# Kernel optimization log

Measured on AMD Instinct MI355X. Metric: run time of the kernel, lower is better.

Reference implementation:

```python
import jax, jax.numpy as jnp
import numpy as np

ROPE_BASE = 10000.0
NEG = -1e9

def _rope_tables(N, head_dim, dtype):
    # freq buffer: angles[pos, i] = pos / base^(2i/head_dim), i over half dim
    inv = 1.0 / (ROPE_BASE ** (jnp.arange(0, head_dim, 2, dtype=jnp.float32) / head_dim))
    ang = jnp.arange(N, dtype=jnp.float32)[:, None] * inv[None, :]  # (N, hd/2)
    return jnp.cos(ang).astype(dtype), jnp.sin(ang).astype(dtype)

def _apply_rope(t, cos, sin):
    # t: (B, h, N, hd); rotate-half style
    hd = t.shape[-1]
    t1, t2 = t[..., : hd // 2], t[..., hd // 2 :]
    c = cos[None, None]  # (1,1,N,hd/2)
    s = sin[None, None]
    return jnp.concatenate([t1 * c - t2 * s, t1 * s + t2 * c], axis=-1)


def setup_inputs() -> dict:
    key = jax.random.key(0)
    B, N, D, h = 2, 2048, 2048, 16
    ks = jax.random.split(key, 5)
    x = jax.random.normal(ks[0], (B, N, D), dtype=jnp.float32)
    Wqkv = jax.random.normal(ks[1], (3 * D, D), dtype=jnp.float32) * 0.02
    Wproj = jax.random.normal(ks[2], (D, D), dtype=jnp.float32) * 0.02
    bproj = jax.random.normal(ks[3], (D,), dtype=jnp.float32) * 0.02
    L = jax.random.randint(ks[4], (B,), 1, N + 1, dtype=jnp.int32)
    return {"x": x, "Wqkv": Wqkv, "Wproj": Wproj, "bproj": bproj, "L": L, "n_heads": 16}


def reference(x, Wqkv, Wproj, bproj, L, n_heads):
    B, N, D = x.shape
    hd = D // n_heads
    scale = 1.0 / jnp.sqrt(jnp.asarray(hd, dtype=x.dtype))

    # fused QKV projection (no bias)
    qkv = jnp.einsum('bnd,ed->bne', x, Wqkv)  # (B, N, 3D)
    q, k, v = jnp.split(qkv, 3, axis=-1)
    # (B, N, h*hd) -> (B, h, N, hd)
    def heads(t):
        return t.reshape(B, N, n_heads, hd).transpose(0, 2, 1, 3)
    q, k, v = heads(q), heads(k), heads(v)

    cos, sin = _rope_tables(N, hd, x.dtype)
    q = _apply_rope(q, cos, sin)
    k = _apply_rope(k, cos, sin)

    # causal + key-padding mask (pos < L valid)
    pos = jnp.arange(N)
    causal = pos[:, None] >= pos[None, :]                    # (N, N)
    key_valid = pos[None, :] < L[:, None]                    # (B, N)
    mask = causal[None, None] & key_valid[:, None, None, :]  # (B,1,N,N)

    scores = jnp.einsum('bhqd,bhkd->bhqk', q, k) * scale
    scores = jnp.where(mask, scores, NEG)
    attn = jax.nn.softmax(scores, axis=-1)
    out = jnp.einsum('bhqk,bhkd->bhqd', attn, v)             # (B,h,N,hd)
    out = out.transpose(0, 2, 1, 3).reshape(B, N, D)
    return jnp.einsum('bnd,ed->bne', out, Wproj) + bproj
```

## Files before the change

kernel.cpp:

```cpp
#include <hip/hip_runtime.h>
#include <hip/hip_bf16.h>


typedef unsigned short u16;
typedef short bf16x8 __attribute__((ext_vector_type(8)));
typedef unsigned short u16x8 __attribute__((ext_vector_type(8)));
typedef float f32x4 __attribute__((ext_vector_type(4)));

#define MFMA16(a, b, c) __builtin_amdgcn_mfma_f32_16x16x32_bf16((a), (b), (c), 0, 0, 0)

__device__ __forceinline__ float b2f(u16 u) { return __uint_as_float(((unsigned)u) << 16); }
__device__ __forceinline__ u16 f2b(float f) {
    unsigned x = __float_as_uint(f);
    return (u16)((x + 0x7fffu + ((x >> 16) & 1u)) >> 16);
}
__device__ __forceinline__ void gload16(const u16* g, u16* lds) {
    __builtin_amdgcn_global_load_lds((__attribute__((address_space(1))) void*)g,
                                     (__attribute__((address_space(3))) void*)lds,
                                     16, 0, 0);
}

__global__ __launch_bounds__(256) void cvt_bf16(const float* __restrict__ in,
                                                u16* __restrict__ out) {
    size_t i = (size_t)blockIdx.x * 256 + threadIdx.x;
    float4 a = ((const float4*)in)[2 * i];
    float4 b = ((const float4*)in)[2 * i + 1];
    u16x8 o;
    o[0] = f2b(a.x); o[1] = f2b(a.y); o[2] = f2b(a.z); o[3] = f2b(a.w);
    o[4] = f2b(b.x); o[5] = f2b(b.y); o[6] = f2b(b.z); o[7] = f2b(b.w);
    ((u16x8*)out)[i] = o;
}

__global__ __launch_bounds__(256) void rope_tables_k(float* __restrict__ cosT,
                                                     float* __restrict__ sinT) {
    int idx = blockIdx.x * 256 + threadIdx.x;
    int n = idx >> 6, i = idx & 63;
    float inv = powf(10000.0f, -(float)(2 * i) / 128.0f);
    float ang = (float)n * inv;
    cosT[idx] = cosf(ang);
    sinT[idx] = sinf(ang);
}

template <int OUTF32>
__global__ __launch_bounds__(256, 2) void gemm_nt(const u16* __restrict__ A,
                                                  const u16* __restrict__ B,
                                                  void* __restrict__ Cv,
                                                  const float* __restrict__ bias,
                                                  int M, int Ncols, int K) {
    __shared__ u16 As[128 * 64];
    __shared__ u16 Bs[128 * 64];
    const int tx = threadIdx.x;
    const int w = tx >> 6, l = tx & 63;
    const int fr = l & 15, fg = l >> 4;
    const int wr = w >> 1, wc = w & 1;
    const long row0 = (long)blockIdx.x * 128;
    const long col0 = (long)blockIdx.y * 128;
    f32x4 acc[4][4] = {};
    const int nk = K >> 6;
    int rs[4], ss[4];
#pragma unroll
    for (int i = 0; i < 4; ++i) {
        int c = i * 256 + tx;
        rs[i] = c >> 3;
        ss[i] = (c & 7) ^ ((c >> 3) & 7);
    }
    for (int kt = 0; kt < nk; ++kt) {
        const long k0 = (long)kt << 6;
        __syncthreads();
#pragma unroll
        for (int i = 0; i < 4; ++i)
            gload16(A + (row0 + rs[i]) * K + k0 + ss[i] * 8, &As[(i * 256 + w * 64) * 8]);
#pragma unroll
        for (int i = 0; i < 4; ++i)
            gload16(B + (col0 + rs[i]) * K + k0 + ss[i] * 8, &Bs[(i * 256 + w * 64) * 8]);
        __syncthreads();
#pragma unroll
        for (int kk = 0; kk < 2; ++kk) {
            bf16x8 af[4], bfv[4];
#pragma unroll
            for (int m = 0; m < 4; ++m) {
                int r = wr * 64 + m * 16 + fr;
                af[m] = *(const bf16x8*)&As[r * 64 + (((kk * 4 + fg) ^ (r & 7)) << 3)];
            }
#pragma unroll
            for (int n = 0; n < 4; ++n) {
                int r = wc * 64 + n * 16 + fr;
                bfv[n] = *(const bf16x8*)&Bs[r * 64 + (((kk * 4 + fg) ^ (r & 7)) << 3)];
            }
#pragma unroll
            for (int m = 0; m < 4; ++m)
#pragma unroll
                for (int n = 0; n < 4; ++n) acc[m][n] = MFMA16(af[m], bfv[n], acc[m][n]);
        }
    }
#pragma unroll
    for (int m = 0; m < 4; ++m) {
#pragma unroll
        for (int n = 0; n < 4; ++n) {
#pragma unroll
            for (int r = 0; r < 4; ++r) {
                long row = row0 + wr * 64 + m * 16 + fg * 4 + r;
                long col = col0 + wc * 64 + n * 16 + fr;
                float v = acc[m][n][r];
                if (OUTF32) {
                    ((float*)Cv)[row * Ncols + col] = v + bias[col];
                } else {
                    ((u16*)Cv)[row * Ncols + col] = f2b(v);
                }
            }
        }
    }
}

__global__ __launch_bounds__(256) void rope_transpose_k(
    const u16* __restrict__ qkv, const float* __restrict__ cosT,
    const float* __restrict__ sinT, u16* __restrict__ Q, u16* __restrict__ Ko,
    u16* __restrict__ VT) {
    const int bh = blockIdx.y, b = bh >> 4, h = bh & 15;
    const int n0 = blockIdx.x << 7;
    const int tx = threadIdx.x;
    __shared__ u16 vbuf[128][136];
    const float SCALE = 0.08838834764831844f;
#pragma unroll
    for (int pass = 0; pass < 4; ++pass) {
        const int rr = pass * 32 + (tx >> 3);
        const int p = tx & 7;
        const int n = n0 + rr;
        const u16* src = qkv + ((size_t)(b * 2048 + n)) * 6144 + h * 128;
        float c[8], s[8];
#pragma unroll
        for (int j = 0; j < 8; ++j) {
            c[j] = cosT[n * 64 + p * 8 + j];
            s[j] = sinT[n * 64 + p * 8 + j];
        }
        {
            u16x8 t1 = *(const u16x8*)&src[p * 8];
            u16x8 t2 = *(const u16x8*)&src[64 + p * 8];
            u16x8 o1, o2;
#pragma unroll
            for (int j = 0; j < 8; ++j) {
                float a = b2f(t1[j]), bb = b2f(t2[j]);
                o1[j] = f2b((a * c[j] - bb * s[j]) * SCALE);
                o2[j] = f2b((a * s[j] + bb * c[j]) * SCALE);
            }
            u16* dst = Q + ((size_t)bh * 2048 + n) * 128;
            *(u16x8*)&dst[p * 8] = o1;
            *(u16x8*)&dst[64 + p * 8] = o2;
        }
        {
            u16x8 t1 = *(const u16x8*)&src[2048 + p * 8];
            u16x8 t2 = *(const u16x8*)&src[2048 + 64 + p * 8];
            u16x8 o1, o2;
#pragma unroll
            for (int j = 0; j < 8; ++j) {
                float a = b2f(t1[j]), bb = b2f(t2[j]);
                o1[j] = f2b(a * c[j] - bb * s[j]);
                o2[j] = f2b(a * s[j] + bb * c[j]);
            }
            u16* dst = Ko + ((size_t)bh * 2048 + n) * 128;
            *(u16x8*)&dst[p * 8] = o1;
            *(u16x8*)&dst[64 + p * 8] = o2;
        }
    }
#pragma unroll
    for (int i = 0; i < 8; ++i) {
        int cid = i * 256 + tx;
        int rr = cid >> 4, cc = cid & 15;
        *(u16x8*)&vbuf[rr][cc * 8] =
            *(const u16x8*)&qkv[((size_t)(b * 2048 + n0 + rr)) * 6144 + 4096 + h * 128 + cc * 8];
    }
    __syncthreads();
#pragma unroll
    for (int i = 0; i < 8; ++i) {
        int cid = i * 256 + tx;
        int j = cid >> 4, nc = cid & 15;
        u16x8 o;
#pragma unroll
        for (int e = 0; e < 8; ++e) o[e] = vbuf[nc * 8 + e][j];
        *(u16x8*)&VT[((size_t)bh * 128 + j) * 2048 + n0 + nc * 8] = o;
    }
}

__global__ __launch_bounds__(256, 2) void attn_k(const u16* __restrict__ Q,
                                                 const u16* __restrict__ K,
                                                 const u16* __restrict__ VT,
                                                 u16* __restrict__ O,
                                                 const int* __restrict__ L) {
    const int bh = blockIdx.y, b = bh >> 4, h = bh & 15;
    const int qx = blockIdx.x;
    const int qb0 = qx << 6, qb1 = (31 - qx) << 6;
    const int tx = threadIdx.x;
    const int w = tx >> 6, l = tx & 63;
    const int fr = l & 15, fg = l >> 4;
    const int Lb = L[b];
    __shared__ u16 Ks[2][64 * 128];
    __shared__ u16 Vs[2][128 * 64];
    __shared__ u16 Ps[4][16 * 72];
    const u16* Qh = Q + (size_t)bh * 2048 * 128;
    const u16* Kh = K + (size_t)bh * 2048 * 128;
    const u16* Vh = VT + (size_t)bh * 128 * 2048;
    bf16x8 aq0[4], aq1[4];
#pragma unroll
    for (int kc = 0; kc < 4; ++kc) {
        aq0[kc] = *(const bf16x8*)&Qh[(size_t)(qb0 + w * 16 + fr) * 128 + kc * 32 + fg * 8];
        aq1[kc] = *(const bf16x8*)&Qh[(size_t)(qb1 + w * 16 + fr) * 128 + kc * 32 + fg * 8];
    }
    f32x4 accO0[8] = {}, accO1[8] = {};
    float mr0[4] = {-1e30f, -1e30f, -1e30f, -1e30f};
    float mr1[4] = {-1e30f, -1e30f, -1e30f, -1e30f};
    float sr0[4] = {0.f, 0.f, 0.f, 0.f};
    float sr1[4] = {0.f, 0.f, 0.f, 0.f};
    const int kmax = min(qb1 + 63, Lb - 1);
    const int nkt = (kmax >> 6) + 1;

    auto stage_tile = [&](int kt0, int buf) {
#pragma unroll
        for (int i = 0; i < 4; ++i) {
            int c = i * 256 + tx;
            int row = c >> 4, cp = c & 15;
            gload16(Kh + (size_t)(kt0 + row) * 128 + ((cp ^ (row & 7)) << 3),
                    &Ks[buf][(i * 256 + w * 64) * 8]);
        }
#pragma unroll
        for (int i = 0; i < 4; ++i) {
            int c = i * 256 + tx;
            int row = c >> 3, cp = c & 7;
            gload16(Vh + (size_t)row * 2048 + kt0 + ((cp ^ (row & 7)) << 3),
                    &Vs[buf][(i * 256 + w * 64) * 8]);
        }
    };

    auto do_strip = [&](const bf16x8 (&aqs)[4], float (&mr)[4], float (&sr)[4],
                        f32x4 (&aO)[8], int qgb, int kt0, const u16* Ksb,
                        const u16* Vsb) {
        f32x4 accS[4];
#pragma unroll
        for (int st = 0; st < 4; ++st) {
            f32x4 z = {0.f, 0.f, 0.f, 0.f};
            accS[st] = z;
            int key = st * 16 + fr;
#pragma unroll
            for (int kc = 0; kc < 4; ++kc) {
                bf16x8 bk = *(const bf16x8*)&Ksb[key * 128 + (((kc * 4 + fg) ^ (key & 7)) << 3)];
                accS[st] = MFMA16(aqs[kc], bk, accS[st]);
            }
        }
        float sv[4][4];
#pragma unroll
        for (int st = 0; st < 4; ++st)
#pragma unroll
            for (int r = 0; r < 4; ++r) {
                int key = kt0 + st * 16 + fr;
                int qg = qgb + fg * 4 + r;
                sv[st][r] = (key <= qg && key < Lb) ? accS[st][r] : -1e30f;
            }
        float alpha[4], pr[4][4];
#pragma unroll
        for (int r = 0; r < 4; ++r) {
            float lm = fmaxf(fmaxf(sv[0][r], sv[1][r]), fmaxf(sv[2][r], sv[3][r]));
            lm = fmaxf(lm, __shfl_xor(lm, 1));
            lm = fmaxf(lm, __shfl_xor(lm, 2));
            lm = fmaxf(lm, __shfl_xor(lm, 4));
            lm = fmaxf(lm, __shfl_xor(lm, 8));
            float mn = fmaxf(mr[r], lm);
            alpha[r] = exp2f((mr[r] - mn) * 1.44269504f);
            float ls = 0.f;
#pragma unroll
            for (int st = 0; st < 4; ++st) {
                float p = exp2f((sv[st][r] - mn) * 1.44269504f);
                pr[st][r] = p;
                ls += p;
            }
            ls += __shfl_xor(ls, 1);
            ls += __shfl_xor(ls, 2);
            ls += __shfl_xor(ls, 4);
            ls += __shfl_xor(ls, 8);
            sr[r] = sr[r] * alpha[r] + ls;
            mr[r] = mn;
        }
#pragma unroll
        for (int n = 0; n < 8; ++n)
#pragma unroll
            for (int r = 0; r < 4; ++r) aO[n][r] *= alpha[r];
#pragma unroll
        for (int st = 0; st < 4; ++st)
#pragma unroll
            for (int r = 0; r < 4; ++r)
                Ps[w][(fg * 4 + r) * 72 + st * 16 + fr] = f2b(pr[st][r]);
#pragma unroll
        for (int ks = 0; ks < 2; ++ks) {
            bf16x8 ap = *(const bf16x8*)&Ps[w][fr * 72 + ks * 32 + fg * 8];
#pragma unroll
            for (int n = 0; n < 8; ++n) {
                int d = n * 16 + fr;
                bf16x8 bv = *(const bf16x8*)&Vsb[d * 64 + (((ks * 4 + fg) ^ (d & 7)) << 3)];
                aO[n] = MFMA16(ap, bv, aO[n]);
            }
        }
    };

    stage_tile(0, 0);
    int cur = 0;
    for (int kt = 0; kt < nkt; ++kt) {
        const int kt0 = kt << 6;
        __syncthreads();
        if (kt + 1 < nkt) stage_tile((kt + 1) << 6, cur ^ 1);
        if (kt <= qx)
            do_strip(aq0, mr0, sr0, accO0, qb0 + w * 16, kt0, Ks[cur], Vs[cur]);
        do_strip(aq1, mr1, sr1, accO1, qb1 + w * 16, kt0, Ks[cur], Vs[cur]);
        cur ^= 1;
    }
    float inv0[4], inv1[4];
#pragma unroll
    for (int r = 0; r < 4; ++r) {
        inv0[r] = 1.0f / sr0[r];
        inv1[r] = 1.0f / sr1[r];
    }
#pragma unroll
    for (int n = 0; n < 8; ++n)
#pragma unroll
        for (int r = 0; r < 4; ++r) {
            int d = n * 16 + fr;
            int q0 = qb0 + w * 16 + fg * 4 + r;
            int q1 = qb1 + w * 16 + fg * 4 + r;
            O[((size_t)(b * 2048 + q0)) * 2048 + h * 128 + d] = f2b(accO0[n][r] * inv0[r]);
            O[((size_t)(b * 2048 + q1)) * 2048 + h * 128 + d] = f2b(accO1[n][r] * inv1[r]);
        }
}

extern "C" void kernel_launch(void* const* d_in, const int* in_sizes, int n_in,
                              void* d_out, int out_size, void* d_ws, size_t ws_size,
                              hipStream_t stream) {
    const float* x = (const float*)d_in[0];
    const float* Wqkv = (const float*)d_in[1];
    const float* Wproj = (const float*)d_in[2];
    const float* bproj = (const float*)d_in[3];
    const int* L = (const int*)d_in[4];
    float* out = (float*)d_out;

    char* p = (char*)d_ws;
    u16* xbf = (u16*)(p + 0);
    u16* wqkvbf = (u16*)(p + 16777216);
    u16* wprojbf = (u16*)(p + 41943040);
    u16* qkv = (u16*)(p + 50331648);
    u16* Kb = (u16*)(p + 100663296);
    u16* VTb = (u16*)(p + 117440512);
    float* cosT = (float*)(p + 134217728);
    float* sinT = (float*)(p + 134742016);
    u16* Ob = xbf;
    u16* Qb = wqkvbf;

    cvt_bf16<<<4096, 256, 0, stream>>>(x, xbf);
    cvt_bf16<<<6144, 256, 0, stream>>>(Wqkv, wqkvbf);
    cvt_bf16<<<2048, 256, 0, stream>>>(Wproj, wprojbf);
    rope_tables_k<<<512, 256, 0, stream>>>(cosT, sinT);
    gemm_nt<0><<<dim3(32, 48), 256, 0, stream>>>(xbf, wqkvbf, qkv, nullptr, 4096, 6144, 2048);
    rope_transpose_k<<<dim3(16, 32), 256, 0, stream>>>(qkv, cosT, sinT, Qb, Kb, VTb);
    attn_k<<<dim3(16, 32), 256, 0, stream>>>(Qb, Kb, VTb, Ob, L);
    gemm_nt<1><<<dim3(32, 16), 256, 0, stream>>>(Ob, wprojbf, out, bproj, 4096, 2048, 2048);
}
```

Measured before the change: 259.6 us.

## Widen attention blocks to 128-row q tiles with 512 threads and interleaved strips

Each attention block now handles two 128-row query strips with 8 waves, so every staged K/V tile serves twice as many queries. The two strips' QK and PV MFMAs are interleaved per wave, and K/V fragment loads are shared between them. Masking is skipped on fully visible tiles, strips are skipped per wave once past the causal edge, and s_setprio raises priority around the MFMA sections. In exchange the grid has half as many blocks (256), which may leave the device underfilled, and the larger Ps buffer adds LDS pressure.

```diff
diff --git a/kernel.cpp b/kernel.cpp
--- a/kernel.cpp
+++ b/kernel.cpp
@@ -181,79 +181,73 @@
     }
 }
 
-__global__ __launch_bounds__(256, 2) void attn_k(const u16* __restrict__ Q,
-                                                 const u16* __restrict__ K,
-                                                 const u16* __restrict__ VT,
-                                                 u16* __restrict__ O,
-                                                 const int* __restrict__ L) {
+__global__ __launch_bounds__(512) __attribute__((amdgpu_waves_per_eu(2, 2)))
+void attn_k(const u16* __restrict__ Q, const u16* __restrict__ K,
+            const u16* __restrict__ VT, u16* __restrict__ O,
+            const int* __restrict__ L) {
     const int bh = blockIdx.y, b = bh >> 4, h = bh & 15;
     const int qx = blockIdx.x;
-    const int qb0 = qx << 6, qb1 = (31 - qx) << 6;
+    const int qb0 = qx << 7, qb1 = (15 - qx) << 7;
     const int tx = threadIdx.x;
     const int w = tx >> 6, l = tx & 63;
     const int fr = l & 15, fg = l >> 4;
     const int Lb = L[b];
+    const int rb0 = qb0 + w * 16, rb1 = qb1 + w * 16;
     __shared__ u16 Ks[2][64 * 128];
     __shared__ u16 Vs[2][128 * 64];
-    __shared__ u16 Ps[4][16 * 72];
+    __shared__ u16 Ps[8][32 * 72];
     const u16* Qh = Q + (size_t)bh * 2048 * 128;
     const u16* Kh = K + (size_t)bh * 2048 * 128;
     const u16* Vh = VT + (size_t)bh * 128 * 2048;
     bf16x8 aq0[4], aq1[4];
 #pragma unroll
     for (int kc = 0; kc < 4; ++kc) {
-        aq0[kc] = *(const bf16x8*)&Qh[(size_t)(qb0 + w * 16 + fr) * 128 + kc * 32 + fg * 8];
-        aq1[kc] = *(const bf16x8*)&Qh[(size_t)(qb1 + w * 16 + fr) * 128 + kc * 32 + fg * 8];
+        aq0[kc] = *(const bf16x8*)&Qh[(size_t)(rb0 + fr) * 128 + kc * 32 + fg * 8];
+        aq1[kc] = *(const bf16x8*)&Qh[(size_t)(rb1 + fr) * 128 + kc * 32 + fg * 8];
     }
     f32x4 accO0[8] = {}, accO1[8] = {};
     float mr0[4] = {-1e30f, -1e30f, -1e30f, -1e30f};
     float mr1[4] = {-1e30f, -1e30f, -1e30f, -1e30f};
     float sr0[4] = {0.f, 0.f, 0.f, 0.f};
     float sr1[4] = {0.f, 0.f, 0.f, 0.f};
-    const int kmax = min(qb1 + 63, Lb - 1);
+    const int kmax = min(qb1 + 127, Lb - 1);
     const int nkt = (kmax >> 6) + 1;
 
     auto stage_tile = [&](int kt0, int buf) {
 #pragma unroll
-        for (int i = 0; i < 4; ++i) {
-            int c = i * 256 + tx;
+        for (int i = 0; i < 2; ++i) {
+            int c = i * 512 + tx;
             int row = c >> 4, cp = c & 15;
             gload16(Kh + (size_t)(kt0 + row) * 128 + ((cp ^ (row & 7)) << 3),
-                    &Ks[buf][(i * 256 + w * 64) * 8]);
-        }
-#pragma unroll
-        for (int i = 0; i < 4; ++i) {
-            int c = i * 256 + tx;
+                    &Ks[buf][(i * 512 + w * 64) * 8]);
+        }
+#pragma unroll
+        for (int i = 0; i < 2; ++i) {
+            int c = i * 512 + tx;
             int row = c >> 3, cp = c & 7;
             gload16(Vh + (size_t)row * 2048 + kt0 + ((cp ^ (row & 7)) << 3),
-                    &Vs[buf][(i * 256 + w * 64) * 8]);
+                    &Vs[buf][(i * 512 + w * 64) * 8]);
         }
     };
 
-    auto do_strip = [&](const bf16x8 (&aqs)[4], float (&mr)[4], float (&sr)[4],
-                        f32x4 (&aO)[8], int qgb, int kt0, const u16* Ksb,
-                        const u16* Vsb) {
-        f32x4 accS[4];
-#pragma unroll
-        for (int st = 0; st < 4; ++st) {
-            f32x4 z = {0.f, 0.f, 0.f, 0.f};
-            accS[st] = z;
-            int key = st * 16 + fr;
-#pragma unroll
-            for (int kc = 0; kc < 4; ++kc) {
-                bf16x8 bk = *(const bf16x8*)&Ksb[key * 128 + (((kc * 4 + fg) ^ (key & 7)) << 3)];
-                accS[st] = MFMA16(aqs[kc], bk, accS[st]);
-            }
-        }
+    auto softmax_store = [&](f32x4 (&s)[4], float (&mr)[4], float (&sr)[4],
+                             f32x4 (&aO)[8], int rb, int kt0, int prow) {
         float sv[4][4];
-#pragma unroll
-        for (int st = 0; st < 4; ++st)
-#pragma unroll
-            for (int r = 0; r < 4; ++r) {
-                int key = kt0 + st * 16 + fr;
-                int qg = qgb + fg * 4 + r;
-                sv[st][r] = (key <= qg && key < Lb) ? accS[st][r] : -1e30f;
-            }
+        if ((kt0 + 63 <= rb) && (kt0 + 63 < Lb)) {
+#pragma unroll
+            for (int st = 0; st < 4; ++st)
+#pragma unroll
+                for (int r = 0; r < 4; ++r) sv[st][r] = s[st][r];
+        } else {
+#pragma unroll
+            for (int st = 0; st < 4; ++st)
+#pragma unroll
+                for (int r = 0; r < 4; ++r) {
+                    int key = kt0 + st * 16 + fr;
+                    int qg = rb + fg * 4 + r;
+                    sv[st][r] = (key <= qg && key < Lb) ? s[st][r] : -1e30f;
+                }
+        }
         float alpha[4], pr[4][4];
 #pragma unroll
         for (int r = 0; r < 4; ++r) {
@@ -286,17 +280,7 @@
         for (int st = 0; st < 4; ++st)
 #pragma unroll
             for (int r = 0; r < 4; ++r)
-                Ps[w][(fg * 4 + r) * 72 + st * 16 + fr] = f2b(pr[st][r]);
-#pragma unroll
-        for (int ks = 0; ks < 2; ++ks) {
-            bf16x8 ap = *(const bf16x8*)&Ps[w][fr * 72 + ks * 32 + fg * 8];
-#pragma unroll
-            for (int n = 0; n < 8; ++n) {
-                int d = n * 16 + fr;
-                bf16x8 bv = *(const bf16x8*)&Vsb[d * 64 + (((ks * 4 + fg) ^ (d & 7)) << 3)];
-                aO[n] = MFMA16(ap, bv, aO[n]);
-            }
-        }
+                Ps[w][(prow + fg * 4 + r) * 72 + st * 16 + fr] = f2b(pr[st][r]);
     };
 
     stage_tile(0, 0);
@@ -305,9 +289,42 @@
         const int kt0 = kt << 6;
         __syncthreads();
         if (kt + 1 < nkt) stage_tile((kt + 1) << 6, cur ^ 1);
-        if (kt <= qx)
-            do_strip(aq0, mr0, sr0, accO0, qb0 + w * 16, kt0, Ks[cur], Vs[cur]);
-        do_strip(aq1, mr1, sr1, accO1, qb1 + w * 16, kt0, Ks[cur], Vs[cur]);
+        const u16* Ksb = Ks[cur];
+        const u16* Vsb = Vs[cur];
+        const bool a0 = (kt0 <= rb0 + 15);
+        const bool a1 = (kt0 <= rb1 + 15);
+        f32x4 s0[4] = {}, s1[4] = {};
+        __builtin_amdgcn_s_setprio(1);
+#pragma unroll
+        for (int st = 0; st < 4; ++st) {
+            int key = st * 16 + fr;
+#pragma unroll
+            for (int kc = 0; kc < 4; ++kc) {
+                bf16x8 bk = *(const bf16x8*)&Ksb[key * 128 + (((kc * 4 + fg) ^ (key & 7)) << 3)];
+                if (a0) s0[st] = MFMA16(aq0[kc], bk, s0[st]);
+                if (a1) s1[st] = MFMA16(aq1[kc], bk, s1[st]);
+            }
+        }
+        __builtin_amdgcn_s_setprio(0);
+        if (a0) softmax_store(s0, mr0, sr0, accO0, rb0, kt0, 0);
+        if (a1) softmax_store(s1, mr1, sr1, accO1, rb1, kt0, 16);
+        if (a0 || a1) {
+            __builtin_amdgcn_s_setprio(1);
+#pragma unroll
+            for (int ks = 0; ks < 2; ++ks) {
+                bf16x8 ap0, ap1;
+                if (a0) ap0 = *(const bf16x8*)&Ps[w][fr * 72 + ks * 32 + fg * 8];
+                if (a1) ap1 = *(const bf16x8*)&Ps[w][(16 + fr) * 72 + ks * 32 + fg * 8];
+#pragma unroll
+                for (int n = 0; n < 8; ++n) {
+                    int d = n * 16 + fr;
+                    bf16x8 bv = *(const bf16x8*)&Vsb[d * 64 + (((ks * 4 + fg) ^ (d & 7)) << 3)];
+                    if (a0) accO0[n] = MFMA16(ap0, bv, accO0[n]);
+                    if (a1) accO1[n] = MFMA16(ap1, bv, accO1[n]);
+                }
+            }
+            __builtin_amdgcn_s_setprio(0);
+        }
         cur ^= 1;
     }
     float inv0[4], inv1[4];
@@ -321,8 +338,8 @@
 #pragma unroll
         for (int r = 0; r < 4; ++r) {
             int d = n * 16 + fr;
-            int q0 = qb0 + w * 16 + fg * 4 + r;
-            int q1 = qb1 + w * 16 + fg * 4 + r;
+            int q0 = rb0 + fg * 4 + r;
+            int q1 = rb1 + fg * 4 + r;
             O[((size_t)(b * 2048 + q0)) * 2048 + h * 128 + d] = f2b(accO0[n][r] * inv0[r]);
             O[((size_t)(b * 2048 + q1)) * 2048 + h * 128 + d] = f2b(accO1[n][r] * inv1[r]);
         }
@@ -356,6 +373,6 @@
     rope_tables_k<<<512, 256, 0, stream>>>(cosT, sinT);
     gemm_nt<0><<<dim3(32, 48), 256, 0, stream>>>(xbf, wqkvbf, qkv, nullptr, 4096, 6144, 2048);
     rope_transpose_k<<<dim3(16, 32), 256, 0, stream>>>(qkv, cosT, sinT, Qb, Kb, VTb);
-    attn_k<<<dim3(16, 32), 256, 0, stream>>>(Qb, Kb, VTb, Ob, L);
+    attn_k<<<dim3(8, 32), 512, 0, stream>>>(Qb, Kb, VTb, Ob, L);
     gemm_nt<1><<<dim3(32, 16), 256, 0, stream>>>(Ob, wprojbf, out, bproj, 4096, 2048, 2048);
 }
```

New measurement: 289.8 us. +11.7%, slower.

## Fuse RoPE and V transpose into QKV GEMM epilogue; skip mask on interior tiles

Applied to the files above, without the earlier changes.

The QKV projection GEMM now stages its output tile in shared memory and applies RoPE and scaling directly, writing Q, K and transposed V. This removes the intermediate qkv buffer round-trip and a separate kernel launch. The attention kernel also skips per-element causal and padding mask evaluation for key tiles that lie fully inside the valid region. The cost is a heavier GEMM epilogue with an extra LDS pass and syncs.

```diff
diff --git a/kernel.cpp b/kernel.cpp
--- a/kernel.cpp
+++ b/kernel.cpp
@@ -41,12 +41,117 @@
     sinT[idx] = sinf(ang);
 }
 
-template <int OUTF32>
-__global__ __launch_bounds__(256, 2) void gemm_nt(const u16* __restrict__ A,
-                                                  const u16* __restrict__ B,
-                                                  void* __restrict__ Cv,
-                                                  const float* __restrict__ bias,
-                                                  int M, int Ncols, int K) {
+__global__ __launch_bounds__(256, 2) void gemm1_fused(
+    const u16* __restrict__ A, const u16* __restrict__ B,
+    const float* __restrict__ cosT, const float* __restrict__ sinT,
+    u16* __restrict__ Q, u16* __restrict__ Ko, u16* __restrict__ VT) {
+    __shared__ u16 smem[17408];
+    u16* As = smem;
+    u16* Bs = smem + 8192;
+    const int K = 2048;
+    const int tx = threadIdx.x;
+    const int w = tx >> 6, l = tx & 63;
+    const int fr = l & 15, fg = l >> 4;
+    const int wr = w >> 1, wc = w & 1;
+    const long row0 = (long)blockIdx.x * 128;
+    const long col0 = (long)blockIdx.y * 128;
+    f32x4 acc[4][4] = {};
+    int rs[4], ss[4];
+#pragma unroll
+    for (int i = 0; i < 4; ++i) {
+        int c = i * 256 + tx;
+        rs[i] = c >> 3;
+        ss[i] = (c & 7) ^ ((c >> 3) & 7);
+    }
+    for (int kt = 0; kt < 32; ++kt) {
+        const long k0 = (long)kt << 6;
+        __syncthreads();
+#pragma unroll
+        for (int i = 0; i < 4; ++i)
+            gload16(A + (row0 + rs[i]) * K + k0 + ss[i] * 8, &As[(i * 256 + w * 64) * 8]);
+#pragma unroll
+        for (int i = 0; i < 4; ++i)
+            gload16(B + (col0 + rs[i]) * K + k0 + ss[i] * 8, &Bs[(i * 256 + w * 64) * 8]);
+        __syncthreads();
+#pragma unroll
+        for (int kk = 0; kk < 2; ++kk) {
+            bf16x8 af[4], bfv[4];
+#pragma unroll
+            for (int m = 0; m < 4; ++m) {
+                int r = wr * 64 + m * 16 + fr;
+                af[m] = *(const bf16x8*)&As[r * 64 + (((kk * 4 + fg) ^ (r & 7)) << 3)];
+            }
+#pragma unroll
+            for (int n = 0; n < 4; ++n) {
+                int r = wc * 64 + n * 16 + fr;
+                bfv[n] = *(const bf16x8*)&Bs[r * 64 + (((kk * 4 + fg) ^ (r & 7)) << 3)];
+            }
+#pragma unroll
+            for (int m = 0; m < 4; ++m)
+#pragma unroll
+                for (int n = 0; n < 4; ++n) acc[m][n] = MFMA16(af[m], bfv[n], acc[m][n]);
+        }
+    }
+    const int sec = blockIdx.y >> 4;
+    const int h = blockIdx.y & 15;
+    const int b = (int)(row0 >> 11);
+    const int n0 = (int)(row0 & 2047);
+    const int bh = b * 16 + h;
+    __syncthreads();
+#pragma unroll
+    for (int m = 0; m < 4; ++m)
+#pragma unroll
+        for (int n = 0; n < 4; ++n)
+#pragma unroll
+            for (int r = 0; r < 4; ++r)
+                smem[(wr * 64 + m * 16 + fg * 4 + r) * 136 + wc * 64 + n * 16 + fr] =
+                    f2b(acc[m][n][r]);
+    __syncthreads();
+    if (sec < 2) {
+        const float SC = (sec == 0) ? 0.08838834764831844f : 1.0f;
+        u16* dstb = (sec == 0 ? Q : Ko) + ((size_t)bh * 2048 + n0) * 128;
+#pragma unroll
+        for (int i = 0; i < 4; ++i) {
+            int cid = i * 256 + tx;
+            int rowl = cid >> 3, g = cid & 7;
+            int d0 = g * 8;
+            int ntok = n0 + rowl;
+            u16x8 t1 = *(const u16x8*)&smem[rowl * 136 + d0];
+            u16x8 t2 = *(const u16x8*)&smem[rowl * 136 + 64 + d0];
+            float4 c1 = *(const float4*)&cosT[ntok * 64 + d0];
+            float4 c2 = *(const float4*)&cosT[ntok * 64 + d0 + 4];
+            float4 s1 = *(const float4*)&sinT[ntok * 64 + d0];
+            float4 s2 = *(const float4*)&sinT[ntok * 64 + d0 + 4];
+            float cc[8] = {c1.x, c1.y, c1.z, c1.w, c2.x, c2.y, c2.z, c2.w};
+            float ssn[8] = {s1.x, s1.y, s1.z, s1.w, s2.x, s2.y, s2.z, s2.w};
+            u16x8 o1, o2;
+#pragma unroll
+            for (int j = 0; j < 8; ++j) {
+                float a = b2f(t1[j]), bb = b2f(t2[j]);
+                o1[j] = f2b((a * cc[j] - bb * ssn[j]) * SC);
+                o2[j] = f2b((a * ssn[j] + bb * cc[j]) * SC);
+            }
+            *(u16x8*)&dstb[(size_t)rowl * 128 + d0] = o1;
+            *(u16x8*)&dstb[(size_t)rowl * 128 + 64 + d0] = o2;
+        }
+    } else {
+#pragma unroll
+        for (int i = 0; i < 8; ++i) {
+            int cid = i * 256 + tx;
+            int d = cid >> 4, g = cid & 15;
+            u16x8 o;
+#pragma unroll
+            for (int e = 0; e < 8; ++e) o[e] = smem[(g * 8 + e) * 136 + d];
+            *(u16x8*)&VT[((size_t)bh * 128 + d) * 2048 + n0 + g * 8] = o;
+        }
+    }
+}
+
+__global__ __launch_bounds__(256, 2) void gemm_nt_f32(const u16* __restrict__ A,
+                                                      const u16* __restrict__ B,
+                                                      float* __restrict__ C,
+                                                      const float* __restrict__ bias,
+                                                      int Ncols, int K) {
     __shared__ u16 As[128 * 64];
     __shared__ u16 Bs[128 * 64];
     const int tx = threadIdx.x;
@@ -94,91 +199,15 @@
         }
     }
 #pragma unroll
-    for (int m = 0; m < 4; ++m) {
-#pragma unroll
-        for (int n = 0; n < 4; ++n) {
+    for (int m = 0; m < 4; ++m)
+#pragma unroll
+        for (int n = 0; n < 4; ++n)
 #pragma unroll
             for (int r = 0; r < 4; ++r) {
                 long row = row0 + wr * 64 + m * 16 + fg * 4 + r;
                 long col = col0 + wc * 64 + n * 16 + fr;
-                float v = acc[m][n][r];
-                if (OUTF32) {
-                    ((float*)Cv)[row * Ncols + col] = v + bias[col];
-                } else {
-                    ((u16*)Cv)[row * Ncols + col] = f2b(v);
-                }
-            }
-        }
-    }
-}
-
-__global__ __launch_bounds__(256) void rope_transpose_k(
-    const u16* __restrict__ qkv, const float* __restrict__ cosT,
-    const float* __restrict__ sinT, u16* __restrict__ Q, u16* __restrict__ Ko,
-    u16* __restrict__ VT) {
-    const int bh = blockIdx.y, b = bh >> 4, h = bh & 15;
-    const int n0 = blockIdx.x << 7;
-    const int tx = threadIdx.x;
-    __shared__ u16 vbuf[128][136];
-    const float SCALE = 0.08838834764831844f;
-#pragma unroll
-    for (int pass = 0; pass < 4; ++pass) {
-        const int rr = pass * 32 + (tx >> 3);
-        const int p = tx & 7;
-        const int n = n0 + rr;
-        const u16* src = qkv + ((size_t)(b * 2048 + n)) * 6144 + h * 128;
-        float c[8], s[8];
-#pragma unroll
-        for (int j = 0; j < 8; ++j) {
-            c[j] = cosT[n * 64 + p * 8 + j];
-            s[j] = sinT[n * 64 + p * 8 + j];
-        }
-        {
-            u16x8 t1 = *(const u16x8*)&src[p * 8];
-            u16x8 t2 = *(const u16x8*)&src[64 + p * 8];
-            u16x8 o1, o2;
-#pragma unroll
-            for (int j = 0; j < 8; ++j) {
-                float a = b2f(t1[j]), bb = b2f(t2[j]);
-                o1[j] = f2b((a * c[j] - bb * s[j]) * SCALE);
-                o2[j] = f2b((a * s[j] + bb * c[j]) * SCALE);
-            }
-            u16* dst = Q + ((size_t)bh * 2048 + n) * 128;
-            *(u16x8*)&dst[p * 8] = o1;
-            *(u16x8*)&dst[64 + p * 8] = o2;
-        }
-        {
-            u16x8 t1 = *(const u16x8*)&src[2048 + p * 8];
-            u16x8 t2 = *(const u16x8*)&src[2048 + 64 + p * 8];
-            u16x8 o1, o2;
-#pragma unroll
-            for (int j = 0; j < 8; ++j) {
-                float a = b2f(t1[j]), bb = b2f(t2[j]);
-                o1[j] = f2b(a * c[j] - bb * s[j]);
-                o2[j] = f2b(a * s[j] + bb * c[j]);
-            }
-            u16* dst = Ko + ((size_t)bh * 2048 + n) * 128;
-            *(u16x8*)&dst[p * 8] = o1;
-            *(u16x8*)&dst[64 + p * 8] = o2;
-        }
-    }
-#pragma unroll
-    for (int i = 0; i < 8; ++i) {
-        int cid = i * 256 + tx;
-        int rr = cid >> 4, cc = cid & 15;
-        *(u16x8*)&vbuf[rr][cc * 8] =
-            *(const u16x8*)&qkv[((size_t)(b * 2048 + n0 + rr)) * 6144 + 4096 + h * 128 + cc * 8];
-    }
-    __syncthreads();
-#pragma unroll
-    for (int i = 0; i < 8; ++i) {
-        int cid = i * 256 + tx;
-        int j = cid >> 4, nc = cid & 15;
-        u16x8 o;
-#pragma unroll
-        for (int e = 0; e < 8; ++e) o[e] = vbuf[nc * 8 + e][j];
-        *(u16x8*)&VT[((size_t)bh * 128 + j) * 2048 + n0 + nc * 8] = o;
-    }
+                C[row * Ncols + col] = acc[m][n][r] + bias[col];
+            }
 }
 
 __global__ __launch_bounds__(256, 2) void attn_k(const u16* __restrict__ Q,
@@ -246,14 +275,21 @@
             }
         }
         float sv[4][4];
-#pragma unroll
-        for (int st = 0; st < 4; ++st)
-#pragma unroll
-            for (int r = 0; r < 4; ++r) {
-                int key = kt0 + st * 16 + fr;
-                int qg = qgb + fg * 4 + r;
-                sv[st][r] = (key <= qg && key < Lb) ? accS[st][r] : -1e30f;
-            }
+        if ((kt0 + 63 <= qgb) && (kt0 + 63 < Lb)) {
+#pragma unroll
+            for (int st = 0; st < 4; ++st)
+#pragma unroll
+                for (int r = 0; r < 4; ++r) sv[st][r] = accS[st][r];
+        } else {
+#pragma unroll
+            for (int st = 0; st < 4; ++st)
+#pragma unroll
+                for (int r = 0; r < 4; ++r) {
+                    int key = kt0 + st * 16 + fr;
+                    int qg = qgb + fg * 4 + r;
+                    sv[st][r] = (key <= qg && key < Lb) ? accS[st][r] : -1e30f;
+                }
+        }
         float alpha[4], pr[4][4];
 #pragma unroll
         for (int r = 0; r < 4; ++r) {
@@ -342,20 +378,18 @@
     u16* xbf = (u16*)(p + 0);
     u16* wqkvbf = (u16*)(p + 16777216);
     u16* wprojbf = (u16*)(p + 41943040);
-    u16* qkv = (u16*)(p + 50331648);
+    u16* Qb = (u16*)(p + 50331648);
     u16* Kb = (u16*)(p + 100663296);
     u16* VTb = (u16*)(p + 117440512);
     float* cosT = (float*)(p + 134217728);
     float* sinT = (float*)(p + 134742016);
     u16* Ob = xbf;
-    u16* Qb = wqkvbf;
 
     cvt_bf16<<<4096, 256, 0, stream>>>(x, xbf);
     cvt_bf16<<<6144, 256, 0, stream>>>(Wqkv, wqkvbf);
     cvt_bf16<<<2048, 256, 0, stream>>>(Wproj, wprojbf);
     rope_tables_k<<<512, 256, 0, stream>>>(cosT, sinT);
-    gemm_nt<0><<<dim3(32, 48), 256, 0, stream>>>(xbf, wqkvbf, qkv, nullptr, 4096, 6144, 2048);
-    rope_transpose_k<<<dim3(16, 32), 256, 0, stream>>>(qkv, cosT, sinT, Qb, Kb, VTb);
+    gemm1_fused<<<dim3(32, 48), 256, 0, stream>>>(xbf, wqkvbf, cosT, sinT, Qb, Kb, VTb);
     attn_k<<<dim3(16, 32), 256, 0, stream>>>(Qb, Kb, VTb, Ob, L);
-    gemm_nt<1><<<dim3(32, 16), 256, 0, stream>>>(Ob, wprojbf, out, bproj, 4096, 2048, 2048);
-}
+    gemm_nt_f32<<<dim3(32, 16), 256, 0, stream>>>(Ob, wprojbf, out, bproj, 2048, 2048);
+}
```

Measured after the change: 245.5 us. 5.4% less time.
